# Kernel tuning notes

Hardware: AMD Instinct MI355X
Metric: run time of the kernel (lower is better)

## Reference

```python
import jax, jax.numpy as jnp
import numpy as np
import math


def _omega_np(nrows: int, ncols: int, rng: np.random.RandomState) -> np.ndarray:
    # Block-orthogonal random feature matrix, transposed to (ncols, nrows)
    nblocks = int(nrows / ncols)
    blocks = []
    for _ in range(nblocks):
        q, _ = np.linalg.qr(rng.normal(size=(ncols, ncols)))
        blocks.append(q.T)
    missing = nrows - nblocks * ncols
    if missing > 0:
        q, _ = np.linalg.qr(rng.normal(size=(ncols, ncols)))
        blocks.append(q.T[:missing])
    norm = np.linalg.norm(rng.normal(size=(nrows, ncols)), axis=1, keepdims=True)
    return (norm * np.vstack(blocks)).T  # (ncols, nrows) = (dim_qk, m)


def setup_inputs() -> dict:
    N, DIM_QK, DIM_V, M = 262144, 128, 128, 256
    key = jax.random.key(0)
    kq, kk, kv = jax.random.split(key, 3)
    Q = jax.random.normal(kq, (N, DIM_QK), dtype=jnp.float32)
    K = jax.random.normal(kk, (N, DIM_QK), dtype=jnp.float32)
    V = jax.random.normal(kv, (N, DIM_V), dtype=jnp.float32)
    omega = jnp.asarray(_omega_np(M, DIM_QK, np.random.RandomState(0)), dtype=jnp.float32)
    return {"Q": Q, "K": K, "V": V, "omega": omega}


def _phi(X, omega, is_query: bool, eps: float = 1e-4):
    d = X.shape[-1]
    m = omega.shape[-1]
    U = jnp.matmul(X / d ** 0.25, omega)                       # [N, m]
    h = jnp.sum(X * X, axis=-1, keepdims=True) / (2.0 * d ** 0.5)
    if is_query:
        maximum = jnp.max(U, axis=-1, keepdims=True)
    else:
        maximum = jnp.max(U)
    return (jnp.exp(U - h - maximum) + eps) / math.sqrt(m)


def reference(Q, K, V, omega):
    eps = 1e-8
    Qp = _phi(Q, omega, True)    # [N, m]
    Kp = _phi(K, omega, False)   # [N, m]
    norm = Qp @ jnp.sum(Kp, axis=0) + eps                       # [N]
    # Faithful to einsum('nF,nF,nf->nf', Qp, Kp, V): row-wise dot * V
    w = jnp.sum(Qp * Kp, axis=-1, keepdims=True)                # [N, 1]
    return w * V / norm[:, None]                                # [N, dim_v]
```

## Files before the change

### kernel.cpp

```cpp
#include <hip/hip_runtime.h>
#include <hip/hip_bf16.h>


typedef _Float16 f16x8 __attribute__((ext_vector_type(8)));
typedef float f32x4 __attribute__((ext_vector_type(4)));

#define D_QK 128
#define M_F  256
#define OMS  136

constexpr float D4      = 0.29730177875068026f;
constexpr float H_SCALE = 0.044194173824159216f;

__device__ __forceinline__ unsigned f2key(float f) {
  unsigned b = __float_as_uint(f);
  return (b & 0x80000000u) ? ~b : (b | 0x80000000u);
}
__device__ __forceinline__ float key2f(unsigned k) {
  return (k & 0x80000000u) ? __uint_as_float(k & 0x7fffffffu) : __uint_as_float(~k);
}

__device__ __forceinline__ f32x4 mfma16(f16x8 a, f16x8 b, f32x4 c) {
  return __builtin_amdgcn_mfma_f32_16x16x32_f16(a, b, c, 0, 0, 0);
}

__device__ __forceinline__ void load_frag(const float* __restrict__ row, int ks, int q,
                                          f16x8& a, float& h) {
  const float4* p = (const float4*)(row + ks * 32 + q * 8);
  float4 x0 = p[0], x1 = p[1];
  h += x0.x*x0.x + x0.y*x0.y + x0.z*x0.z + x0.w*x0.w
     + x1.x*x1.x + x1.y*x1.y + x1.z*x1.z + x1.w*x1.w;
  a[0] = (_Float16)(x0.x * D4); a[1] = (_Float16)(x0.y * D4);
  a[2] = (_Float16)(x0.z * D4); a[3] = (_Float16)(x0.w * D4);
  a[4] = (_Float16)(x1.x * D4); a[5] = (_Float16)(x1.y * D4);
  a[6] = (_Float16)(x1.z * D4); a[7] = (_Float16)(x1.w * D4);
}

extern "C" __global__ void k_prep(const float* __restrict__ om, _Float16* __restrict__ omt,
                                  float* __restrict__ S, unsigned* __restrict__ Mkey) {
  int i = blockIdx.x * 256 + threadIdx.x;
  if (i < D_QK * M_F) {
    int m = i >> 7, d = i & 127;
    omt[m * OMS + d] = (_Float16)om[d * M_F + m];
  }
  if (blockIdx.x == 0) {
    S[threadIdx.x] = 0.f;
    if (threadIdx.x == 0) *Mkey = 0u;
  }
}

__global__ __launch_bounds__(256, 4) void k_kstats(
    const float* __restrict__ K, const _Float16* __restrict__ omt,
    float* __restrict__ Lout, float* __restrict__ Pout, unsigned* __restrict__ Mkey) {
  __shared__ _Float16 om_lds[128 * OMS];
  __shared__ float P_lds[4][256];
  __shared__ float red_lds[4];
  int tid = threadIdx.x;
  int w = tid >> 6, lane = tid & 63, q = lane >> 4, c = lane & 15;
  int rb = blockIdx.x * 64 + w * 16;

  const float* krow = K + (size_t)(rb + c) * D_QK;
  f16x8 ak[4];
  float hk = 0.f;
#pragma unroll
  for (int ks = 0; ks < 4; ++ks) load_frag(krow, ks, q, ak[ks], hk);
  hk += __shfl_xor(hk, 16, 64);
  hk += __shfl_xor(hk, 32, 64);
  hk *= H_SCALE;

  const f32x4 zero = {0.f, 0.f, 0.f, 0.f};
  f32x4 cc[16];
#pragma unroll
  for (int t = 0; t < 16; ++t) cc[t] = zero;

  const float4* osrc = (const float4*)omt;
  float4* odst = (float4*)om_lds;
  for (int i = tid; i < 2176; i += 256) odst[i] = osrc[i];
  __syncthreads();
#pragma unroll
  for (int t = 0; t < 8; ++t) {
#pragma unroll
    for (int ks = 0; ks < 4; ++ks) {
      f16x8 b = *(const f16x8*)&om_lds[(t * 16 + c) * OMS + ks * 32 + q * 8];
      cc[t] = mfma16(ak[ks], b, cc[t]);
    }
  }
  __syncthreads();
  for (int i = tid; i < 2176; i += 256) odst[i] = osrc[i + 2176];
  __syncthreads();
#pragma unroll
  for (int t = 8; t < 16; ++t) {
#pragma unroll
    for (int ks = 0; ks < 4; ++ks) {
      f16x8 b = *(const f16x8*)&om_lds[((t - 8) * 16 + c) * OMS + ks * 32 + q * 8];
      cc[t] = mfma16(ak[ks], b, cc[t]);
    }
  }

  float mx = cc[0][0];
#pragma unroll
  for (int t = 0; t < 16; ++t)
    mx = fmaxf(mx, fmaxf(fmaxf(cc[t][0], cc[t][1]), fmaxf(cc[t][2], cc[t][3])));
#pragma unroll
  for (int m = 1; m <= 32; m <<= 1) mx = fmaxf(mx, __shfl_xor(mx, m, 64));
  if (lane == 0) red_lds[w] = mx;
  __syncthreads();
  float Lb = fmaxf(fmaxf(red_lds[0], red_lds[1]), fmaxf(red_lds[2], red_lds[3]));

  float hr[4];
#pragma unroll
  for (int r = 0; r < 4; ++r) hr[r] = __shfl(hk, q * 4 + r, 64);

#pragma unroll
  for (int t = 0; t < 16; ++t) {
    float s = __expf(cc[t][0] - hr[0] - Lb) + __expf(cc[t][1] - hr[1] - Lb)
            + __expf(cc[t][2] - hr[2] - Lb) + __expf(cc[t][3] - hr[3] - Lb);
    s += __shfl_xor(s, 16, 64);
    s += __shfl_xor(s, 32, 64);
    if (q == 0) P_lds[w][t * 16 + c] = s;
  }
  __syncthreads();
  Pout[(size_t)blockIdx.x * 256 + tid] =
      P_lds[0][tid] + P_lds[1][tid] + P_lds[2][tid] + P_lds[3][tid];
  if (tid == 0) {
    Lout[blockIdx.x] = Lb;
    atomicMax(Mkey, f2key(Lb));
  }
}

extern "C" __global__ void k_combine(const float* __restrict__ Lout, const float* __restrict__ Pout,
                                     const unsigned* __restrict__ Mkey, float* __restrict__ Mout,
                                     float* __restrict__ S) {
  float M = key2f(*Mkey);
  if (blockIdx.x == 0 && threadIdx.x == 0) *Mout = M;
  int b0 = blockIdx.x * 32;
  float acc = 0.f;
  for (int i = 0; i < 32; ++i) {
    int b = b0 + i;
    float f = __expf(Lout[b] - M);
    acc += f * Pout[(size_t)b * 256 + threadIdx.x];
  }
  atomicAdd(&S[threadIdx.x], acc);
}

__global__ __launch_bounds__(256, 2) void k_main(
    const float* __restrict__ Q, const float* __restrict__ K, const float* __restrict__ V,
    const _Float16* __restrict__ omt, const float* __restrict__ Sws,
    const float* __restrict__ Mws, float* __restrict__ out, float epsN) {
  __shared__ _Float16 om_lds[128 * OMS];
  __shared__ float S_lds[256];
  __shared__ float scale_lds[64];
  int tid = threadIdx.x;
  int w = tid >> 6, lane = tid & 63, q = lane >> 4, c = lane & 15;
  int rb = blockIdx.x * 64 + w * 16;

  S_lds[tid] = (Sws[tid] + epsN) * 0.0625f;
  float Mglob = *Mws;

  const float* qrow = Q + (size_t)(rb + c) * D_QK;
  const float* krow = K + (size_t)(rb + c) * D_QK;
  f16x8 aq[4], ak[4];
  float hq = 0.f, hk = 0.f;
#pragma unroll
  for (int ks = 0; ks < 4; ++ks) {
    load_frag(qrow, ks, q, aq[ks], hq);
    load_frag(krow, ks, q, ak[ks], hk);
  }
  hq += __shfl_xor(hq, 16, 64); hq += __shfl_xor(hq, 32, 64); hq *= H_SCALE;
  hk += __shfl_xor(hk, 16, 64); hk += __shfl_xor(hk, 32, 64); hk *= H_SCALE;

  const f32x4 zero = {0.f, 0.f, 0.f, 0.f};
  f32x4 cq[16], ck[16];
#pragma unroll
  for (int t = 0; t < 16; ++t) { cq[t] = zero; ck[t] = zero; }

  const float4* osrc = (const float4*)omt;
  float4* odst = (float4*)om_lds;
  for (int i = tid; i < 2176; i += 256) odst[i] = osrc[i];
  __syncthreads();
#pragma unroll
  for (int t = 0; t < 8; ++t) {
#pragma unroll
    for (int ks = 0; ks < 4; ++ks) {
      f16x8 b = *(const f16x8*)&om_lds[(t * 16 + c) * OMS + ks * 32 + q * 8];
      cq[t] = mfma16(aq[ks], b, cq[t]);
      ck[t] = mfma16(ak[ks], b, ck[t]);
    }
  }
  __syncthreads();
  for (int i = tid; i < 2176; i += 256) odst[i] = osrc[i + 2176];
  __syncthreads();
#pragma unroll
  for (int t = 8; t < 16; ++t) {
#pragma unroll
    for (int ks = 0; ks < 4; ++ks) {
      f16x8 b = *(const f16x8*)&om_lds[((t - 8) * 16 + c) * OMS + ks * 32 + q * 8];
      cq[t] = mfma16(aq[ks], b, cq[t]);
      ck[t] = mfma16(ak[ks], b, ck[t]);
    }
  }

  float hqr[4], hkr[4];
#pragma unroll
  for (int r = 0; r < 4; ++r) {
    hqr[r] = __shfl(hq, q * 4 + r, 64);
    hkr[r] = __shfl(hk, q * 4 + r, 64);
  }

#pragma unroll
  for (int r = 0; r < 4; ++r) {
    float mx = cq[0][r];
#pragma unroll
    for (int t = 1; t < 16; ++t) mx = fmaxf(mx, cq[t][r]);
#pragma unroll
    for (int m = 1; m <= 8; m <<= 1) mx = fmaxf(mx, __shfl_xor(mx, m, 64));
    float wsum = 0.f, nsum = 0.f;
#pragma unroll
    for (int t = 0; t < 16; ++t) {
      float qp = __expf(cq[t][r] - hqr[r] - mx) + 1e-4f;
      float kp = __expf(ck[t][r] - hkr[r] - Mglob) + 1e-4f;
      wsum += qp * kp;
      nsum += qp * S_lds[t * 16 + c];
    }
#pragma unroll
    for (int m = 1; m <= 8; m <<= 1) {
      wsum += __shfl_xor(wsum, m, 64);
      nsum += __shfl_xor(nsum, m, 64);
    }
    if (c == 0)
      scale_lds[w * 16 + q * 4 + r] = (wsum * (1.f / 256.f)) / (nsum * 0.0625f + 1e-8f);
  }
  __syncthreads();

  const float4* vsrc = (const float4*)(V + (size_t)blockIdx.x * 64 * D_QK);
  float4* odst4 = (float4*)(out + (size_t)blockIdx.x * 64 * D_QK);
#pragma unroll
  for (int i = 0; i < 8; ++i) {
    int j = tid + i * 256;
    float s = scale_lds[j >> 5];
    float4 v = vsrc[j];
    odst4[j] = make_float4(v.x * s, v.y * s, v.z * s, v.w * s);
  }
}

extern "C" void kernel_launch(void* const* d_in, const int* in_sizes, int n_in,
                              void* d_out, int out_size, void* d_ws, size_t ws_size,
                              hipStream_t stream) {
  const float* Q  = (const float*)d_in[0];
  const float* K  = (const float*)d_in[1];
  const float* V  = (const float*)d_in[2];
  const float* om = (const float*)d_in[3];
  float* out = (float*)d_out;
  int N = in_sizes[0] / D_QK;
  int nblk = N / 64;

  char* ws = (char*)d_ws;
  _Float16* omt = (_Float16*)ws;
  size_t off = (size_t)M_F * OMS * 2;
  float* Lout = (float*)(ws + off);   off += (size_t)nblk * 4;
  float* Pout = (float*)(ws + off);   off += (size_t)nblk * 256 * 4;
  float* S    = (float*)(ws + off);   off += 1024;
  unsigned* Mkey = (unsigned*)(ws + off); off += 16;
  float* Mout = (float*)(ws + off);

  hipLaunchKernelGGL(k_prep, dim3((D_QK * M_F + 255) / 256), dim3(256), 0, stream,
                     om, omt, S, Mkey);
  hipLaunchKernelGGL(k_kstats, dim3(nblk), dim3(256), 0, stream, K, omt, Lout, Pout, Mkey);
  hipLaunchKernelGGL(k_combine, dim3(nblk / 32), dim3(256), 0, stream, Lout, Pout, Mkey, Mout, S);
  hipLaunchKernelGGL(k_main, dim3(nblk), dim3(256), 0, stream, Q, K, V, omt, S, Mout, out,
                     (float)N * 1e-4f);
}
```

Before: 519.2 us.

## Process eight row chunks per block with full omega in LDS and prefetch

```diff
diff --git a/kernel.cpp b/kernel.cpp
--- a/kernel.cpp
+++ b/kernel.cpp
@@ -8,6 +8,8 @@
 #define D_QK 128
 #define M_F  256
 #define OMS  136
+#define CH   8
+#define ROWS_PER_BLK (CH * 64)
 
 constexpr float D4      = 0.29730177875068026f;
 constexpr float H_SCALE = 0.044194173824159216f;
@@ -24,16 +26,32 @@
   return __builtin_amdgcn_mfma_f32_16x16x32_f16(a, b, c, 0, 0, 0);
 }
 
-__device__ __forceinline__ void load_frag(const float* __restrict__ row, int ks, int q,
-                                          f16x8& a, float& h) {
-  const float4* p = (const float4*)(row + ks * 32 + q * 8);
-  float4 x0 = p[0], x1 = p[1];
-  h += x0.x*x0.x + x0.y*x0.y + x0.z*x0.z + x0.w*x0.w
-     + x1.x*x1.x + x1.y*x1.y + x1.z*x1.z + x1.w*x1.w;
-  a[0] = (_Float16)(x0.x * D4); a[1] = (_Float16)(x0.y * D4);
-  a[2] = (_Float16)(x0.z * D4); a[3] = (_Float16)(x0.w * D4);
-  a[4] = (_Float16)(x1.x * D4); a[5] = (_Float16)(x1.y * D4);
-  a[6] = (_Float16)(x1.z * D4); a[7] = (_Float16)(x1.w * D4);
+__device__ __forceinline__ void issue_loads(const float* __restrict__ rowq, float4* buf) {
+#pragma unroll
+  for (int ks = 0; ks < 4; ++ks) {
+    const float4* p = (const float4*)(rowq + ks * 32);
+    buf[2 * ks]     = p[0];
+    buf[2 * ks + 1] = p[1];
+  }
+}
+
+__device__ __forceinline__ void conv_frag(const float4* buf, f16x8* a, float& h) {
+  h = 0.f;
+#pragma unroll
+  for (int ks = 0; ks < 4; ++ks) {
+    float4 x0 = buf[2 * ks], x1 = buf[2 * ks + 1];
+    h += x0.x*x0.x + x0.y*x0.y + x0.z*x0.z + x0.w*x0.w
+       + x1.x*x1.x + x1.y*x1.y + x1.z*x1.z + x1.w*x1.w;
+    f16x8 t;
+    t[0] = (_Float16)(x0.x * D4); t[1] = (_Float16)(x0.y * D4);
+    t[2] = (_Float16)(x0.z * D4); t[3] = (_Float16)(x0.w * D4);
+    t[4] = (_Float16)(x1.x * D4); t[5] = (_Float16)(x1.y * D4);
+    t[6] = (_Float16)(x1.z * D4); t[7] = (_Float16)(x1.w * D4);
+    a[ks] = t;
+  }
+  h += __shfl_xor(h, 16, 64);
+  h += __shfl_xor(h, 32, 64);
+  h *= H_SCALE;
 }
 
 extern "C" __global__ void k_prep(const float* __restrict__ om, _Float16* __restrict__ omt,
@@ -49,72 +67,78 @@
   }
 }
 
-__global__ __launch_bounds__(256, 4) void k_kstats(
+__global__ __launch_bounds__(256, 2) void k_kstats(
     const float* __restrict__ K, const _Float16* __restrict__ omt,
     float* __restrict__ Lout, float* __restrict__ Pout, unsigned* __restrict__ Mkey) {
-  __shared__ _Float16 om_lds[128 * OMS];
+  __shared__ __align__(16) _Float16 om_lds[M_F * OMS];
   __shared__ float P_lds[4][256];
   __shared__ float red_lds[4];
   int tid = threadIdx.x;
   int w = tid >> 6, lane = tid & 63, q = lane >> 4, c = lane & 15;
-  int rb = blockIdx.x * 64 + w * 16;
-
-  const float* krow = K + (size_t)(rb + c) * D_QK;
-  f16x8 ak[4];
-  float hk = 0.f;
-#pragma unroll
-  for (int ks = 0; ks < 4; ++ks) load_frag(krow, ks, q, ak[ks], hk);
-  hk += __shfl_xor(hk, 16, 64);
-  hk += __shfl_xor(hk, 32, 64);
-  hk *= H_SCALE;
-
-  const f32x4 zero = {0.f, 0.f, 0.f, 0.f};
-  f32x4 cc[16];
-#pragma unroll
-  for (int t = 0; t < 16; ++t) cc[t] = zero;
 
   const float4* osrc = (const float4*)omt;
   float4* odst = (float4*)om_lds;
-  for (int i = tid; i < 2176; i += 256) odst[i] = osrc[i];
-  __syncthreads();
-#pragma unroll
-  for (int t = 0; t < 8; ++t) {
-#pragma unroll
-    for (int ks = 0; ks < 4; ++ks) {
-      f16x8 b = *(const f16x8*)&om_lds[(t * 16 + c) * OMS + ks * 32 + q * 8];
-      cc[t] = mfma16(ak[ks], b, cc[t]);
-    }
-  }
-  __syncthreads();
-  for (int i = tid; i < 2176; i += 256) odst[i] = osrc[i + 2176];
-  __syncthreads();
-#pragma unroll
-  for (int t = 8; t < 16; ++t) {
-#pragma unroll
-    for (int ks = 0; ks < 4; ++ks) {
-      f16x8 b = *(const f16x8*)&om_lds[((t - 8) * 16 + c) * OMS + ks * 32 + q * 8];
-      cc[t] = mfma16(ak[ks], b, cc[t]);
-    }
-  }
-
-  float mx = cc[0][0];
-#pragma unroll
-  for (int t = 0; t < 16; ++t)
-    mx = fmaxf(mx, fmaxf(fmaxf(cc[t][0], cc[t][1]), fmaxf(cc[t][2], cc[t][3])));
-#pragma unroll
-  for (int m = 1; m <= 32; m <<= 1) mx = fmaxf(mx, __shfl_xor(mx, m, 64));
-  if (lane == 0) red_lds[w] = mx;
+#pragma unroll
+  for (int i = 0; i < 17; ++i) odst[tid + i * 256] = osrc[tid + i * 256];
+  __syncthreads();
+
+  const float* kbase = K + ((size_t)blockIdx.x * ROWS_PER_BLK + w * 16 + c) * D_QK + q * 8;
+
+  float4 kraw[8];
+  issue_loads(kbase, kraw);
+
+  float Lw = -3.0e38f;
+  float ps[16];
+#pragma unroll
+  for (int t = 0; t < 16; ++t) ps[t] = 0.f;
+
+#pragma unroll 1
+  for (int ch = 0; ch < CH; ++ch) {
+    f16x8 ak[4];
+    float hk;
+    conv_frag(kraw, ak, hk);
+    if (ch + 1 < CH) issue_loads(kbase + (size_t)(ch + 1) * 64 * D_QK, kraw);
+
+    const f32x4 zero = {0.f, 0.f, 0.f, 0.f};
+    f32x4 cc[16];
+#pragma unroll
+    for (int t = 0; t < 16; ++t) cc[t] = zero;
+#pragma unroll
+    for (int t = 0; t < 16; ++t)
+#pragma unroll
+      for (int ks = 0; ks < 4; ++ks) {
+        f16x8 b = *(const f16x8*)&om_lds[(t * 16 + c) * OMS + ks * 32 + q * 8];
+        cc[t] = mfma16(ak[ks], b, cc[t]);
+      }
+
+    float mc = cc[0][0];
+#pragma unroll
+    for (int t = 0; t < 16; ++t)
+      mc = fmaxf(mc, fmaxf(fmaxf(cc[t][0], cc[t][1]), fmaxf(cc[t][2], cc[t][3])));
+#pragma unroll
+    for (int m = 1; m <= 32; m <<= 1) mc = fmaxf(mc, __shfl_xor(mc, m, 64));
+
+    float newL = fmaxf(Lw, mc);
+    float f = __expf(Lw - newL);
+    float hr[4];
+#pragma unroll
+    for (int r = 0; r < 4; ++r) hr[r] = __shfl(hk, q * 4 + r, 64);
+#pragma unroll
+    for (int t = 0; t < 16; ++t) {
+      float s = __expf(cc[t][0] - hr[0] - newL) + __expf(cc[t][1] - hr[1] - newL)
+              + __expf(cc[t][2] - hr[2] - newL) + __expf(cc[t][3] - hr[3] - newL);
+      ps[t] = ps[t] * f + s;
+    }
+    Lw = newL;
+  }
+
+  if (lane == 0) red_lds[w] = Lw;
   __syncthreads();
   float Lb = fmaxf(fmaxf(red_lds[0], red_lds[1]), fmaxf(red_lds[2], red_lds[3]));
-
-  float hr[4];
-#pragma unroll
-  for (int r = 0; r < 4; ++r) hr[r] = __shfl(hk, q * 4 + r, 64);
-
+  float f = __expf(Lw - Lb);
 #pragma unroll
   for (int t = 0; t < 16; ++t) {
-    float s = __expf(cc[t][0] - hr[0] - Lb) + __expf(cc[t][1] - hr[1] - Lb)
-            + __expf(cc[t][2] - hr[2] - Lb) + __expf(cc[t][3] - hr[3] - Lb);
+    float s = ps[t] * f;
     s += __shfl_xor(s, 16, 64);
     s += __shfl_xor(s, 32, 64);
     if (q == 0) P_lds[w][t * 16 + c] = s;
@@ -147,99 +171,93 @@
     const float* __restrict__ Q, const float* __restrict__ K, const float* __restrict__ V,
     const _Float16* __restrict__ omt, const float* __restrict__ Sws,
     const float* __restrict__ Mws, float* __restrict__ out, float epsN) {
-  __shared__ _Float16 om_lds[128 * OMS];
+  __shared__ __align__(16) _Float16 om_lds[M_F * OMS];
   __shared__ float S_lds[256];
-  __shared__ float scale_lds[64];
+  __shared__ float scale_lds[4][16];
   int tid = threadIdx.x;
   int w = tid >> 6, lane = tid & 63, q = lane >> 4, c = lane & 15;
-  int rb = blockIdx.x * 64 + w * 16;
 
   S_lds[tid] = (Sws[tid] + epsN) * 0.0625f;
   float Mglob = *Mws;
 
-  const float* qrow = Q + (size_t)(rb + c) * D_QK;
-  const float* krow = K + (size_t)(rb + c) * D_QK;
-  f16x8 aq[4], ak[4];
-  float hq = 0.f, hk = 0.f;
-#pragma unroll
-  for (int ks = 0; ks < 4; ++ks) {
-    load_frag(qrow, ks, q, aq[ks], hq);
-    load_frag(krow, ks, q, ak[ks], hk);
-  }
-  hq += __shfl_xor(hq, 16, 64); hq += __shfl_xor(hq, 32, 64); hq *= H_SCALE;
-  hk += __shfl_xor(hk, 16, 64); hk += __shfl_xor(hk, 32, 64); hk *= H_SCALE;
-
-  const f32x4 zero = {0.f, 0.f, 0.f, 0.f};
-  f32x4 cq[16], ck[16];
-#pragma unroll
-  for (int t = 0; t < 16; ++t) { cq[t] = zero; ck[t] = zero; }
-
   const float4* osrc = (const float4*)omt;
   float4* odst = (float4*)om_lds;
-  for (int i = tid; i < 2176; i += 256) odst[i] = osrc[i];
-  __syncthreads();
-#pragma unroll
-  for (int t = 0; t < 8; ++t) {
-#pragma unroll
-    for (int ks = 0; ks < 4; ++ks) {
-      f16x8 b = *(const f16x8*)&om_lds[(t * 16 + c) * OMS + ks * 32 + q * 8];
-      cq[t] = mfma16(aq[ks], b, cq[t]);
-      ck[t] = mfma16(ak[ks], b, ck[t]);
-    }
-  }
-  __syncthreads();
-  for (int i = tid; i < 2176; i += 256) odst[i] = osrc[i + 2176];
-  __syncthreads();
-#pragma unroll
-  for (int t = 8; t < 16; ++t) {
-#pragma unroll
-    for (int ks = 0; ks < 4; ++ks) {
-      f16x8 b = *(const f16x8*)&om_lds[((t - 8) * 16 + c) * OMS + ks * 32 + q * 8];
-      cq[t] = mfma16(aq[ks], b, cq[t]);
-      ck[t] = mfma16(ak[ks], b, ck[t]);
-    }
-  }
-
-  float hqr[4], hkr[4];
-#pragma unroll
-  for (int r = 0; r < 4; ++r) {
-    hqr[r] = __shfl(hq, q * 4 + r, 64);
-    hkr[r] = __shfl(hk, q * 4 + r, 64);
-  }
-
-#pragma unroll
-  for (int r = 0; r < 4; ++r) {
-    float mx = cq[0][r];
-#pragma unroll
-    for (int t = 1; t < 16; ++t) mx = fmaxf(mx, cq[t][r]);
-#pragma unroll
-    for (int m = 1; m <= 8; m <<= 1) mx = fmaxf(mx, __shfl_xor(mx, m, 64));
-    float wsum = 0.f, nsum = 0.f;
-#pragma unroll
-    for (int t = 0; t < 16; ++t) {
-      float qp = __expf(cq[t][r] - hqr[r] - mx) + 1e-4f;
-      float kp = __expf(ck[t][r] - hkr[r] - Mglob) + 1e-4f;
-      wsum += qp * kp;
-      nsum += qp * S_lds[t * 16 + c];
-    }
-#pragma unroll
-    for (int m = 1; m <= 8; m <<= 1) {
-      wsum += __shfl_xor(wsum, m, 64);
-      nsum += __shfl_xor(nsum, m, 64);
-    }
-    if (c == 0)
-      scale_lds[w * 16 + q * 4 + r] = (wsum * (1.f / 256.f)) / (nsum * 0.0625f + 1e-8f);
-  }
-  __syncthreads();
-
-  const float4* vsrc = (const float4*)(V + (size_t)blockIdx.x * 64 * D_QK);
-  float4* odst4 = (float4*)(out + (size_t)blockIdx.x * 64 * D_QK);
-#pragma unroll
-  for (int i = 0; i < 8; ++i) {
-    int j = tid + i * 256;
-    float s = scale_lds[j >> 5];
-    float4 v = vsrc[j];
-    odst4[j] = make_float4(v.x * s, v.y * s, v.z * s, v.w * s);
+#pragma unroll
+  for (int i = 0; i < 17; ++i) odst[tid + i * 256] = osrc[tid + i * 256];
+  __syncthreads();
+
+  size_t rb0 = ((size_t)blockIdx.x * ROWS_PER_BLK + w * 16 + c) * D_QK + q * 8;
+  const float* qbase = Q + rb0;
+  const float* kbase = K + rb0;
+
+  float4 qraw[8], kraw[8];
+  issue_loads(qbase, qraw);
+  issue_loads(kbase, kraw);
+
+#pragma unroll 1
+  for (int ch = 0; ch < CH; ++ch) {
+    f16x8 aq[4], ak[4];
+    float hq, hk;
+    conv_frag(qraw, aq, hq);
+    conv_frag(kraw, ak, hk);
+    if (ch + 1 < CH) {
+      issue_loads(qbase + (size_t)(ch + 1) * 64 * D_QK, qraw);
+      issue_loads(kbase + (size_t)(ch + 1) * 64 * D_QK, kraw);
+    }
+
+    const f32x4 zero = {0.f, 0.f, 0.f, 0.f};
+    f32x4 cq[16], ck[16];
+#pragma unroll
+    for (int t = 0; t < 16; ++t) { cq[t] = zero; ck[t] = zero; }
+#pragma unroll
+    for (int t = 0; t < 16; ++t)
+#pragma unroll
+      for (int ks = 0; ks < 4; ++ks) {
+        f16x8 b = *(const f16x8*)&om_lds[(t * 16 + c) * OMS + ks * 32 + q * 8];
+        cq[t] = mfma16(aq[ks], b, cq[t]);
+        ck[t] = mfma16(ak[ks], b, ck[t]);
+      }
+
+    float hqr[4], hkr[4];
+#pragma unroll
+    for (int r = 0; r < 4; ++r) {
+      hqr[r] = __shfl(hq, q * 4 + r, 64);
+      hkr[r] = __shfl(hk, q * 4 + r, 64);
+    }
+
+#pragma unroll
+    for (int r = 0; r < 4; ++r) {
+      float mx = cq[0][r];
+#pragma unroll
+      for (int t = 1; t < 16; ++t) mx = fmaxf(mx, cq[t][r]);
+#pragma unroll
+      for (int m = 1; m <= 8; m <<= 1) mx = fmaxf(mx, __shfl_xor(mx, m, 64));
+      float wsum = 0.f, nsum = 0.f;
+#pragma unroll
+      for (int t = 0; t < 16; ++t) {
+        float qp = __expf(cq[t][r] - hqr[r] - mx) + 1e-4f;
+        float kp = __expf(ck[t][r] - hkr[r] - Mglob) + 1e-4f;
+        wsum += qp * kp;
+        nsum += qp * S_lds[t * 16 + c];
+      }
+#pragma unroll
+      for (int m = 1; m <= 8; m <<= 1) {
+        wsum += __shfl_xor(wsum, m, 64);
+        nsum += __shfl_xor(nsum, m, 64);
+      }
+      if (c == 0)
+        scale_lds[w][q * 4 + r] = (wsum * (1.f / 256.f)) / (nsum * 0.0625f + 1e-8f);
+    }
+    size_t vbase = ((size_t)blockIdx.x * ROWS_PER_BLK + ch * 64 + w * 16) * D_QK;
+    const float4* vsrc = (const float4*)(V + vbase);
+    float4* odst4 = (float4*)(out + vbase);
+#pragma unroll
+    for (int i = 0; i < 8; ++i) {
+      int j = i * 64 + lane;
+      float s = scale_lds[w][j >> 5];
+      float4 v = vsrc[j];
+      odst4[j] = make_float4(v.x * s, v.y * s, v.z * s, v.w * s);
+    }
   }
 }
 
@@ -252,7 +270,7 @@
   const float* om = (const float*)d_in[3];
   float* out = (float*)d_out;
   int N = in_sizes[0] / D_QK;
-  int nblk = N / 64;
+  int nblk = N / ROWS_PER_BLK;
 
   char* ws = (char*)d_ws;
   _Float16* omt = (_Float16*)ws;
```

Result: slower. 813.9 us (+56.8%).
